# Kernel tuning notes

Hardware: AMD Instinct MI355X
Metric: run time of the kernel (lower is better)

Reference implementation:

```python
import jax, jax.numpy as jnp
import numpy as np

B, T = 2, 2048
D_MODEL, D_HIDDEN = 1024, 2048
N_EXPERTS, TOP_K = 8, 2
N_TOKENS = B * T
CAPACITY = 2 * N_TOKENS * TOP_K // N_EXPERTS  # 4096


def setup_inputs() -> dict:
    key = jax.random.key(0)
    k_x, k_rw, k_w, k_v, k_o = jax.random.split(key, 5)
    x = jax.random.normal(k_x, (B, T, D_MODEL), jnp.float32)
    # router: nn.Linear(d_model, n_experts) -> weight [E, D], bias [E]
    router_w = jax.random.normal(k_rw, (N_EXPERTS, D_MODEL), jnp.float32) * D_MODEL ** -0.5
    router_b = jnp.zeros((N_EXPERTS,), jnp.float32)
    # stacked expert params, matching SwiGLU init scales
    W = jax.random.normal(k_w, (N_EXPERTS, D_MODEL, D_HIDDEN), jnp.float32) * D_MODEL ** -0.5
    V = jax.random.normal(k_v, (N_EXPERTS, D_MODEL, D_HIDDEN), jnp.float32) * D_MODEL ** -0.5
    W_out = jax.random.normal(k_o, (N_EXPERTS, D_HIDDEN, D_MODEL), jnp.float32) * D_HIDDEN ** -0.5
    return {"x": x, "router_w": router_w, "router_b": router_b, "W": W, "V": V, "W_out": W_out}


def reference(x, router_w, router_b, W, V, W_out):
    Bq, Tq, D = x.shape
    N = Bq * Tq
    x_flat = x.reshape(N, D)

    # token-level top-k routing
    router_logits = x_flat @ router_w.T + router_b            # [N, E]
    top_vals, top_ids = jax.lax.top_k(router_logits, TOP_K)   # [N, K]
    top_probs = jax.nn.softmax(top_vals, axis=-1)             # [N, K]

    # pad row N: gathers with fill index N read zeros / contribute zero weight
    x_pad = jnp.concatenate([x_flat, jnp.zeros((1, D), x_flat.dtype)], axis=0)
    probs_pad = jnp.concatenate([top_probs, jnp.zeros((1, TOP_K), top_probs.dtype)], axis=0)

    out = jnp.zeros((N + 1, D), x_flat.dtype)
    for e in range(N_EXPERTS):  # static small loop over experts
        tok, slot = jnp.nonzero(top_ids == e, size=CAPACITY, fill_value=(N, 0))
        w = probs_pad[tok, slot][:, None]     # [C, 1], zero for padding slots
        xin = x_pad[tok]                      # [C, D] gather
        a = xin @ W[e]                        # [C, H]
        b = xin @ V[e]                        # [C, H]
        y = (a * (b * jax.nn.sigmoid(b))) @ W_out[e]  # SwiGLU: a * swish(b) -> [C, D]
        out = out.at[tok].add(y * w)          # weighted scatter-add
    return out[:N].reshape(Bq, Tq, D)
```

## Files before the change

kernel.cpp:

```cpp
#include <hip/hip_runtime.h>
#include <cstdint>
#include <cstddef>

#define N_TOK 4096
#define DM    1024
#define DH    2048
#define NE    8
#define NSLOT 8192

typedef short bf16x8_t __attribute__((ext_vector_type(8)));
typedef float f32x4    __attribute__((ext_vector_type(4)));
typedef unsigned short u16x8 __attribute__((ext_vector_type(8)));

__device__ __forceinline__ unsigned short f2bf(float f) {
  union { float f; unsigned int u; } v; v.f = f;
  unsigned int u = v.u;
  u += 0x7fffu + ((u >> 16) & 1u);
  return (unsigned short)(u >> 16);
}

__device__ __forceinline__ float bf2f(unsigned short h) {
  union { unsigned int u; float f; } v; v.u = ((unsigned int)h) << 16;
  return v.f;
}

#define GLD16(gp, lp)                                                          \
  __builtin_amdgcn_global_load_lds(                                            \
      (const __attribute__((address_space(1))) void*)(gp),                     \
      (__attribute__((address_space(3))) void*)(lp), 16, 0, 0)

__device__ __forceinline__ int expert_off(const int* __restrict__ counts, int e, int* cnt) {
  int off = 0, s = 0;
#pragma unroll
  for (int i = 0; i < NE; i++) { if (i == e) off = s; s += counts[i]; }
  *cnt = counts[e];
  return off;
}

__global__ __launch_bounds__(256) void k_transpose(
    const float* __restrict__ W, const float* __restrict__ V,
    const float* __restrict__ Wout, unsigned short* __restrict__ B1t,
    unsigned short* __restrict__ B2t, int* __restrict__ counts) {
  if (blockIdx.z == 0 && blockIdx.x == 0 && blockIdx.y == 0 && threadIdx.x < NE)
    counts[threadIdx.x] = 0;

  const int z = blockIdx.z;
  const float* s;
  unsigned short* d;
  int R, C, xt, yt;
  if (z < 16) {
    const int e = z & 7;
    s = ((z < 8) ? W : V) + (size_t)e * DM * DH;
    d = B1t + (size_t)e * 4096 * DM + (size_t)((z < 8) ? 0 : DH) * DM;
    R = DM; C = DH; xt = blockIdx.x; yt = blockIdx.y;
  } else {
    const int e = z - 16;
    s = Wout + (size_t)e * DH * DM;
    d = B2t + (size_t)e * DM * DH;
    R = DH; C = DM;
    const int flat = blockIdx.x * 16 + blockIdx.y;
    xt = flat & 15; yt = flat >> 4;
  }
  const int c0 = xt * 64, r0 = yt * 64;
  __shared__ float tile[64][65];
  const int t = threadIdx.x;
  {
    const int cc = (t & 15) * 4;
#pragma unroll
    for (int j = 0; j < 4; j++) {
      const int r = (t >> 4) + j * 16;
      const float4 v = *(const float4*)(s + (size_t)(r0 + r) * C + c0 + cc);
      tile[r][cc + 0] = v.x; tile[r][cc + 1] = v.y;
      tile[r][cc + 2] = v.z; tile[r][cc + 3] = v.w;
    }
  }
  __syncthreads();
  {
    const int r8 = (t & 7) * 8;
#pragma unroll
    for (int j = 0; j < 2; j++) {
      const int c = (t >> 3) + j * 32;
      u16x8 o;
#pragma unroll
      for (int i = 0; i < 8; i++) o[i] = f2bf(tile[r8 + i][c]);
      *(u16x8*)(d + (size_t)(c0 + c) * R + r0 + r8) = o;
    }
  }
}

__global__ __launch_bounds__(256) void k_router(
    const float* __restrict__ x, const float* __restrict__ rw,
    const float* __restrict__ rb, int* __restrict__ counts,
    int* __restrict__ meta_e, int* __restrict__ meta_idx,
    float* __restrict__ meta_p) {
  const int wv = threadIdx.x >> 6;
  const int l  = threadIdx.x & 63;
  const int tk = blockIdx.x * 4 + wv;
  const float* xr = x + (size_t)tk * DM;

  float acc[NE];
#pragma unroll
  for (int e = 0; e < NE; e++) acc[e] = 0.f;
#pragma unroll 4
  for (int i = 0; i < DM / 64; i++) {
    const float xv = xr[i * 64 + l];
#pragma unroll
    for (int e = 0; e < NE; e++) acc[e] += xv * rw[e * DM + i * 64 + l];
  }
#pragma unroll
  for (int off = 32; off > 0; off >>= 1) {
#pragma unroll
    for (int e = 0; e < NE; e++) acc[e] += __shfl_xor(acc[e], off);
  }
#pragma unroll
  for (int e = 0; e < NE; e++) acc[e] += rb[e];

  float v0 = -1e30f; int e0 = 0;
#pragma unroll
  for (int e = 0; e < NE; e++) { if (acc[e] > v0) { v0 = acc[e]; e0 = e; } }
  float v1 = -1e30f; int e1 = 0;
#pragma unroll
  for (int e = 0; e < NE; e++) { if (e != e0 && acc[e] > v1) { v1 = acc[e]; e1 = e; } }
  const float p0 = 1.0f / (1.0f + __expf(v1 - v0));
  const float p1 = 1.0f - p0;

  if (l == 0) {
    const int i0 = atomicAdd(&counts[e0], 1);
    const int i1 = atomicAdd(&counts[e1], 1);
    meta_e[tk * 2 + 0] = e0;  meta_e[tk * 2 + 1] = e1;
    meta_idx[tk * 2 + 0] = i0; meta_idx[tk * 2 + 1] = i1;
    meta_p[tk * 2 + 0] = p0;  meta_p[tk * 2 + 1] = p1;
  }
}

__global__ __launch_bounds__(256) void k_gather(
    const float* __restrict__ x, const int* __restrict__ meta_e,
    const int* __restrict__ meta_idx, const int* __restrict__ counts,
    unsigned short* __restrict__ Xg) {
  const int tk = blockIdx.x;
  int offs[NE];
  { int s = 0;
#pragma unroll
    for (int e = 0; e < NE; e++) { offs[e] = s; s += counts[e]; } }
  const int s0 = tk * 2, s1 = s0 + 1;
  const int g0 = offs[meta_e[s0]] + meta_idx[s0];
  const int g1 = offs[meta_e[s1]] + meta_idx[s1];
  const float4 v = ((const float4*)(x + (size_t)tk * DM))[threadIdx.x];
  ushort4 o;
  o.x = f2bf(v.x); o.y = f2bf(v.y); o.z = f2bf(v.z); o.w = f2bf(v.w);
  *(ushort4*)(Xg + (size_t)g0 * DM + threadIdx.x * 4) = o;
  *(ushort4*)(Xg + (size_t)g1 * DM + threadIdx.x * 4) = o;
}

__global__ __launch_bounds__(256, 2) void k_gemm1(
    const unsigned short* __restrict__ Xg, const unsigned short* __restrict__ B1t,
    unsigned short* __restrict__ G, const int* __restrict__ counts) {
  const int e = blockIdx.z;
  int cnt;
  const int off = expert_off(counts, e, &cnt);
  const int mt = blockIdx.y;
  if (mt * 128 >= cnt) return;
  const int h0 = blockIdx.x * 128;
  const int row_base = off + mt * 128;

  __shared__ unsigned short As[2][128 * 32];
  __shared__ unsigned short Ws[2][128 * 32];
  __shared__ unsigned short Vs[2][128 * 32];

  const int t = threadIdx.x;
  const int l = t & 63;
  const int w = t >> 6;
  const int wm = (w >> 1) * 64;
  const int wn = (w & 1) * 64;
  const int lr = l & 15;
  const int kq = (l >> 4) * 8;

  const unsigned short* Bw = B1t + ((size_t)e * 4096 + h0) * DM;
  const unsigned short* Bv = Bw + (size_t)DH * DM;

  const int c0 = t, c1 = t + 256;
  const int r0 = c0 >> 2, r1 = c1 >> 2;
  const int k0s = ((c0 & 3) ^ ((r0 >> 1) & 3)) << 3;
  const int k1s = ((c1 & 3) ^ ((r1 >> 1) & 3)) << 3;
  const size_t aoff0 = (size_t)min(row_base + r0, NSLOT - 1) * DM + k0s;
  const size_t aoff1 = (size_t)min(row_base + r1, NSLOT - 1) * DM + k1s;
  const size_t boff0 = (size_t)r0 * DM + k0s;
  const size_t boff1 = (size_t)r1 * DM + k1s;

#define STG1(buf, kk)                                                          \
  do {                                                                         \
    GLD16(Xg + aoff0 + (kk), &As[buf][c0 * 8]);                                \
    GLD16(Xg + aoff1 + (kk), &As[buf][c1 * 8]);                                \
    GLD16(Bw + boff0 + (kk), &Ws[buf][c0 * 8]);                                \
    GLD16(Bw + boff1 + (kk), &Ws[buf][c1 * 8]);                                \
    GLD16(Bv + boff0 + (kk), &Vs[buf][c0 * 8]);                                \
    GLD16(Bv + boff1 + (kk), &Vs[buf][c1 * 8]);                                \
  } while (0)

  f32x4 acc_a[4][4], acc_b[4][4];
  const f32x4 z4 = {0.f, 0.f, 0.f, 0.f};
#pragma unroll
  for (int i = 0; i < 4; i++)
#pragma unroll
    for (int j = 0; j < 4; j++) { acc_a[i][j] = z4; acc_b[i][j] = z4; }

  STG1(0, 0);
  __syncthreads();

  const int NS = DM / 32;
  for (int s = 0; s < NS; s++) {
    const int cur = s & 1;
    bf16x8_t af[4], wf[4], vf[4];
#pragma unroll
    for (int mi = 0; mi < 4; mi++) {
      const int row = wm + mi * 16 + lr;
      af[mi] = *(const bf16x8_t*)&As[cur][(row * 32 + kq) ^ (((row >> 1) & 3) << 3)];
    }
#pragma unroll
    for (int ni = 0; ni < 4; ni++) {
      const int row = wn + ni * 16 + lr;
      const int idx = (row * 32 + kq) ^ (((row >> 1) & 3) << 3);
      wf[ni] = *(const bf16x8_t*)&Ws[cur][idx];
      vf[ni] = *(const bf16x8_t*)&Vs[cur][idx];
    }
    if (s + 1 < NS) STG1(cur ^ 1, (s + 1) * 32);
#pragma unroll
    for (int mi = 0; mi < 4; mi++)
#pragma unroll
      for (int ni = 0; ni < 4; ni++) {
        acc_a[mi][ni] = __builtin_amdgcn_mfma_f32_16x16x32_bf16(af[mi], wf[ni], acc_a[mi][ni], 0, 0, 0);
        acc_b[mi][ni] = __builtin_amdgcn_mfma_f32_16x16x32_bf16(af[mi], vf[ni], acc_b[mi][ni], 0, 0, 0);
      }
    __syncthreads();
  }
#undef STG1

  const int q4 = (l >> 4) * 4;
#pragma unroll
  for (int mi = 0; mi < 4; mi++) {
#pragma unroll
    for (int r = 0; r < 4; r++) {
      const int mloc = mt * 128 + wm + mi * 16 + q4 + r;
      if (mloc >= cnt) continue;
      unsigned short* grow = G + (size_t)(off + mloc) * DH;
#pragma unroll
      for (int ni = 0; ni < 4; ni++) {
        const int h = h0 + wn + ni * 16 + lr;
        const float a = acc_a[mi][ni][r];
        const float b = acc_b[mi][ni][r];
        const float sgl = b / (1.0f + __expf(-b));
        grow[h] = f2bf(a * sgl);
      }
    }
  }
}

__global__ __launch_bounds__(256, 2) void k_gemm2(
    const unsigned short* __restrict__ G, const unsigned short* __restrict__ B2t,
    unsigned short* __restrict__ Y, const int* __restrict__ counts) {
  const int z = blockIdx.z;
  const int e = z & 7;
  const int half = z >> 3;
  int cnt;
  const int off = expert_off(counts, e, &cnt);
  const int mt = blockIdx.y;
  if (mt * 128 >= cnt) return;
  const int n0 = blockIdx.x * 128;
  const int row_base = off + mt * 128;
  const int kbase = half * 1024;

  __shared__ unsigned short As[2][128 * 32];
  __shared__ unsigned short Bs[2][128 * 32];

  const int t = threadIdx.x;
  const int l = t & 63;
  const int w = t >> 6;
  const int wm = (w >> 1) * 64;
  const int wn = (w & 1) * 64;
  const int lr = l & 15;
  const int kq = (l >> 4) * 8;

  const unsigned short* Bp = B2t + ((size_t)e * DM + n0) * DH;

  const int c0 = t, c1 = t + 256;
  const int r0 = c0 >> 2, r1 = c1 >> 2;
  const int k0s = ((c0 & 3) ^ ((r0 >> 1) & 3)) << 3;
  const int k1s = ((c1 & 3) ^ ((r1 >> 1) & 3)) << 3;
  const size_t aoff0 = (size_t)min(row_base + r0, NSLOT - 1) * DH + k0s;
  const size_t aoff1 = (size_t)min(row_base + r1, NSLOT - 1) * DH + k1s;
  const size_t boff0 = (size_t)r0 * DH + k0s;
  const size_t boff1 = (size_t)r1 * DH + k1s;

#define STG2(buf, kk)                                                          \
  do {                                                                         \
    GLD16(G + aoff0 + (kk), &As[buf][c0 * 8]);                                 \
    GLD16(G + aoff1 + (kk), &As[buf][c1 * 8]);                                 \
    GLD16(Bp + boff0 + (kk), &Bs[buf][c0 * 8]);                                \
    GLD16(Bp + boff1 + (kk), &Bs[buf][c1 * 8]);                                \
  } while (0)

  f32x4 acc[4][4];
  const f32x4 z4 = {0.f, 0.f, 0.f, 0.f};
#pragma unroll
  for (int i = 0; i < 4; i++)
#pragma unroll
    for (int j = 0; j < 4; j++) acc[i][j] = z4;

  STG2(0, kbase);
  __syncthreads();

  const int NS = 1024 / 32;
  for (int s = 0; s < NS; s++) {
    const int cur = s & 1;
    bf16x8_t af[4], bf[4];
#pragma unroll
    for (int mi = 0; mi < 4; mi++) {
      const int row = wm + mi * 16 + lr;
      af[mi] = *(const bf16x8_t*)&As[cur][(row * 32 + kq) ^ (((row >> 1) & 3) << 3)];
    }
#pragma unroll
    for (int ni = 0; ni < 4; ni++) {
      const int row = wn + ni * 16 + lr;
      bf[ni] = *(const bf16x8_t*)&Bs[cur][(row * 32 + kq) ^ (((row >> 1) & 3) << 3)];
    }
    if (s + 1 < NS) STG2(cur ^ 1, kbase + (s + 1) * 32);
#pragma unroll
    for (int mi = 0; mi < 4; mi++)
#pragma unroll
      for (int ni = 0; ni < 4; ni++)
        acc[mi][ni] = __builtin_amdgcn_mfma_f32_16x16x32_bf16(af[mi], bf[ni], acc[mi][ni], 0, 0, 0);
    __syncthreads();
  }
#undef STG2

  unsigned short* Yh = Y + (size_t)half * NSLOT * DM;
  const int q4 = (l >> 4) * 4;
#pragma unroll
  for (int mi = 0; mi < 4; mi++) {
#pragma unroll
    for (int r = 0; r < 4; r++) {
      const int mloc = mt * 128 + wm + mi * 16 + q4 + r;
      if (mloc >= cnt) continue;
      unsigned short* yrow = Yh + (size_t)(off + mloc) * DM;
#pragma unroll
      for (int ni = 0; ni < 4; ni++)
        yrow[n0 + wn + ni * 16 + lr] = f2bf(acc[mi][ni][r]);
    }
  }
}

__global__ __launch_bounds__(256) void k_combine(
    const unsigned short* __restrict__ Y, const int* __restrict__ meta_e,
    const int* __restrict__ meta_idx, const float* __restrict__ meta_p,
    const int* __restrict__ counts, float* __restrict__ out) {
  const int tk = blockIdx.x;
  int offs[NE];
  { int s = 0;
#pragma unroll
    for (int e = 0; e < NE; e++) { offs[e] = s; s += counts[e]; } }
  const int s0 = tk * 2, s1 = s0 + 1;
  const int g0 = offs[meta_e[s0]] + meta_idx[s0];
  const int g1 = offs[meta_e[s1]] + meta_idx[s1];
  const float w0 = meta_p[s0], w1 = meta_p[s1];
  const unsigned short* Y1 = Y + (size_t)NSLOT * DM;
  const ushort4 a0 = ((const ushort4*)(Y  + (size_t)g0 * DM))[threadIdx.x];
  const ushort4 a1 = ((const ushort4*)(Y1 + (size_t)g0 * DM))[threadIdx.x];
  const ushort4 b0 = ((const ushort4*)(Y  + (size_t)g1 * DM))[threadIdx.x];
  const ushort4 b1 = ((const ushort4*)(Y1 + (size_t)g1 * DM))[threadIdx.x];
  float4 o;
  o.x = w0 * (bf2f(a0.x) + bf2f(a1.x)) + w1 * (bf2f(b0.x) + bf2f(b1.x));
  o.y = w0 * (bf2f(a0.y) + bf2f(a1.y)) + w1 * (bf2f(b0.y) + bf2f(b1.y));
  o.z = w0 * (bf2f(a0.z) + bf2f(a1.z)) + w1 * (bf2f(b0.z) + bf2f(b1.z));
  o.w = w0 * (bf2f(a0.w) + bf2f(a1.w)) + w1 * (bf2f(b0.w) + bf2f(b1.w));
  ((float4*)(out + (size_t)tk * DM))[threadIdx.x] = o;
}

extern "C" void kernel_launch(void* const* d_in, const int* in_sizes, int n_in,
                              void* d_out, int out_size, void* d_ws, size_t ws_size,
                              hipStream_t stream) {
  const float* x    = (const float*)d_in[0];
  const float* rw   = (const float*)d_in[1];
  const float* rb   = (const float*)d_in[2];
  const float* W    = (const float*)d_in[3];
  const float* V    = (const float*)d_in[4];
  const float* Wout = (const float*)d_in[5];
  float* out = (float*)d_out;

  char* p = (char*)d_ws;
  unsigned short* B1t = (unsigned short*)p; p += (size_t)NE * 4096 * DM * 2;
  unsigned short* Y   = (unsigned short*)B1t;
  unsigned short* B2t = (unsigned short*)p; p += (size_t)NE * DM * DH * 2;
  unsigned short* Xg  = (unsigned short*)p; p += (size_t)NSLOT * DM * 2;
  unsigned short* G   = (unsigned short*)p; p += (size_t)NSLOT * DH * 2;
  int*   counts      = (int*)p;   p += 256;
  int*   meta_e      = (int*)p;   p += (size_t)N_TOK * 2 * 4;
  int*   meta_idx    = (int*)p;   p += (size_t)N_TOK * 2 * 4;
  float* meta_p      = (float*)p; p += (size_t)N_TOK * 2 * 4;

  k_transpose<<<dim3(32, 16, 24), 256, 0, stream>>>(W, V, Wout, B1t, B2t, counts);
  k_router<<<N_TOK / 4, 256, 0, stream>>>(x, rw, rb, counts, meta_e, meta_idx, meta_p);
  k_gather<<<N_TOK, 256, 0, stream>>>(x, meta_e, meta_idx, counts, Xg);
  k_gemm1<<<dim3(DH / 128, NSLOT / 128, NE), 256, 0, stream>>>(Xg, B1t, G, counts);
  k_gemm2<<<dim3(DM / 128, NSLOT / 128, 2 * NE), 256, 0, stream>>>(G, B2t, Y, counts);
  k_combine<<<N_TOK, 256, 0, stream>>>(Y, meta_e, meta_idx, meta_p, counts, out);
}
```

Measured before the change: 501.6 us.

## Use larger transpose tiles, block-local router atomics, and drop split-K in gemm2

The weight transpose kernel now handles 128x64 tiles per block, halving its grid. The router processes 32 tokens per block and aggregates per-expert counts in shared memory before one global atomic per expert, cutting global atomic contention. The second GEMM no longer splits K into two halves, so combine reads one partial output instead of two. This removes the extra Y traffic and the reduction, but halves gemm2's block count, which risks lower occupancy.

```diff
diff --git a/kernel.cpp b/kernel.cpp
--- a/kernel.cpp
+++ b/kernel.cpp
@@ -58,16 +58,16 @@
     s = Wout + (size_t)e * DH * DM;
     d = B2t + (size_t)e * DM * DH;
     R = DH; C = DM;
-    const int flat = blockIdx.x * 16 + blockIdx.y;
+    const int flat = blockIdx.x * 8 + blockIdx.y;
     xt = flat & 15; yt = flat >> 4;
   }
-  const int c0 = xt * 64, r0 = yt * 64;
-  __shared__ float tile[64][65];
+  const int c0 = xt * 64, r0 = yt * 128;
+  __shared__ float tile[128][65];
   const int t = threadIdx.x;
   {
     const int cc = (t & 15) * 4;
 #pragma unroll
-    for (int j = 0; j < 4; j++) {
+    for (int j = 0; j < 8; j++) {
       const int r = (t >> 4) + j * 16;
       const float4 v = *(const float4*)(s + (size_t)(r0 + r) * C + c0 + cc);
       tile[r][cc + 0] = v.x; tile[r][cc + 1] = v.y;
@@ -76,10 +76,11 @@
   }
   __syncthreads();
   {
-    const int r8 = (t & 7) * 8;
-#pragma unroll
-    for (int j = 0; j < 2; j++) {
-      const int c = (t >> 3) + j * 32;
+    const int r8 = (t & 15) * 8;
+    const int cb = t >> 4;
+#pragma unroll
+    for (int pass = 0; pass < 4; pass++) {
+      const int c = cb + pass * 16;
       u16x8 o;
 #pragma unroll
       for (int i = 0; i < 8; i++) o[i] = f2bf(tile[r8 + i][c]);
@@ -88,48 +89,73 @@
   }
 }
 
+#define RTR_TOK 32
 __global__ __launch_bounds__(256) void k_router(
     const float* __restrict__ x, const float* __restrict__ rw,
     const float* __restrict__ rb, int* __restrict__ counts,
     int* __restrict__ meta_e, int* __restrict__ meta_idx,
     float* __restrict__ meta_p) {
+  __shared__ int lcnt[NE];
+  __shared__ int lbase[NE];
+  __shared__ int   tokE[RTR_TOK][2];
+  __shared__ int   tokLi[RTR_TOK][2];
+  __shared__ float tokP[RTR_TOK][2];
+
   const int wv = threadIdx.x >> 6;
   const int l  = threadIdx.x & 63;
-  const int tk = blockIdx.x * 4 + wv;
-  const float* xr = x + (size_t)tk * DM;
-
-  float acc[NE];
-#pragma unroll
-  for (int e = 0; e < NE; e++) acc[e] = 0.f;
+  if (threadIdx.x < NE) lcnt[threadIdx.x] = 0;
+  __syncthreads();
+
+  for (int it = 0; it < RTR_TOK / 4; it++) {
+    const int lt = wv * (RTR_TOK / 4) + it;
+    const int tk = blockIdx.x * RTR_TOK + lt;
+    const float* xr = x + (size_t)tk * DM;
+
+    float acc[NE];
+#pragma unroll
+    for (int e = 0; e < NE; e++) acc[e] = 0.f;
 #pragma unroll 4
-  for (int i = 0; i < DM / 64; i++) {
-    const float xv = xr[i * 64 + l];
-#pragma unroll
-    for (int e = 0; e < NE; e++) acc[e] += xv * rw[e * DM + i * 64 + l];
-  }
-#pragma unroll
-  for (int off = 32; off > 0; off >>= 1) {
-#pragma unroll
-    for (int e = 0; e < NE; e++) acc[e] += __shfl_xor(acc[e], off);
-  }
-#pragma unroll
-  for (int e = 0; e < NE; e++) acc[e] += rb[e];
-
-  float v0 = -1e30f; int e0 = 0;
-#pragma unroll
-  for (int e = 0; e < NE; e++) { if (acc[e] > v0) { v0 = acc[e]; e0 = e; } }
-  float v1 = -1e30f; int e1 = 0;
-#pragma unroll
-  for (int e = 0; e < NE; e++) { if (e != e0 && acc[e] > v1) { v1 = acc[e]; e1 = e; } }
-  const float p0 = 1.0f / (1.0f + __expf(v1 - v0));
-  const float p1 = 1.0f - p0;
-
-  if (l == 0) {
-    const int i0 = atomicAdd(&counts[e0], 1);
-    const int i1 = atomicAdd(&counts[e1], 1);
-    meta_e[tk * 2 + 0] = e0;  meta_e[tk * 2 + 1] = e1;
-    meta_idx[tk * 2 + 0] = i0; meta_idx[tk * 2 + 1] = i1;
-    meta_p[tk * 2 + 0] = p0;  meta_p[tk * 2 + 1] = p1;
+    for (int i = 0; i < DM / 64; i++) {
+      const float xv = xr[i * 64 + l];
+#pragma unroll
+      for (int e = 0; e < NE; e++) acc[e] += xv * rw[e * DM + i * 64 + l];
+    }
+#pragma unroll
+    for (int off = 32; off > 0; off >>= 1) {
+#pragma unroll
+      for (int e = 0; e < NE; e++) acc[e] += __shfl_xor(acc[e], off);
+    }
+#pragma unroll
+    for (int e = 0; e < NE; e++) acc[e] += rb[e];
+
+    float v0 = -1e30f; int e0 = 0;
+#pragma unroll
+    for (int e = 0; e < NE; e++) { if (acc[e] > v0) { v0 = acc[e]; e0 = e; } }
+    float v1 = -1e30f; int e1 = 0;
+#pragma unroll
+    for (int e = 0; e < NE; e++) { if (e != e0 && acc[e] > v1) { v1 = acc[e]; e1 = e; } }
+    const float p0 = 1.0f / (1.0f + __expf(v1 - v0));
+    const float p1 = 1.0f - p0;
+
+    if (l == 0) {
+      const int li0 = atomicAdd(&lcnt[e0], 1);
+      const int li1 = atomicAdd(&lcnt[e1], 1);
+      tokE[lt][0] = e0;  tokE[lt][1] = e1;
+      tokLi[lt][0] = li0; tokLi[lt][1] = li1;
+      tokP[lt][0] = p0;  tokP[lt][1] = p1;
+    }
+  }
+  __syncthreads();
+  if (threadIdx.x < NE)
+    lbase[threadIdx.x] = atomicAdd(&counts[threadIdx.x], lcnt[threadIdx.x]);
+  __syncthreads();
+  if (threadIdx.x < RTR_TOK * 2) {
+    const int lt = threadIdx.x >> 1, k = threadIdx.x & 1;
+    const int tk = blockIdx.x * RTR_TOK + lt;
+    const int e = tokE[lt][k];
+    meta_e[tk * 2 + k] = e;
+    meta_idx[tk * 2 + k] = lbase[e] + tokLi[lt][k];
+    meta_p[tk * 2 + k] = tokP[lt][k];
   }
 }
 
@@ -258,16 +284,13 @@
 __global__ __launch_bounds__(256, 2) void k_gemm2(
     const unsigned short* __restrict__ G, const unsigned short* __restrict__ B2t,
     unsigned short* __restrict__ Y, const int* __restrict__ counts) {
-  const int z = blockIdx.z;
-  const int e = z & 7;
-  const int half = z >> 3;
+  const int e = blockIdx.z;
   int cnt;
   const int off = expert_off(counts, e, &cnt);
   const int mt = blockIdx.y;
   if (mt * 128 >= cnt) return;
   const int n0 = blockIdx.x * 128;
   const int row_base = off + mt * 128;
-  const int kbase = half * 1024;
 
   __shared__ unsigned short As[2][128 * 32];
   __shared__ unsigned short Bs[2][128 * 32];
@@ -306,10 +329,10 @@
 #pragma unroll
     for (int j = 0; j < 4; j++) acc[i][j] = z4;
 
-  STG2(0, kbase);
-  __syncthreads();
-
-  const int NS = 1024 / 32;
+  STG2(0, 0);
+  __syncthreads();
+
+  const int NS = DH / 32;
   for (int s = 0; s < NS; s++) {
     const int cur = s & 1;
     bf16x8_t af[4], bf[4];
@@ -323,7 +346,7 @@
       const int row = wn + ni * 16 + lr;
       bf[ni] = *(const bf16x8_t*)&Bs[cur][(row * 32 + kq) ^ (((row >> 1) & 3) << 3)];
     }
-    if (s + 1 < NS) STG2(cur ^ 1, kbase + (s + 1) * 32);
+    if (s + 1 < NS) STG2(cur ^ 1, (s + 1) * 32);
 #pragma unroll
     for (int mi = 0; mi < 4; mi++)
 #pragma unroll
@@ -333,7 +356,6 @@
   }
 #undef STG2
 
-  unsigned short* Yh = Y + (size_t)half * NSLOT * DM;
   const int q4 = (l >> 4) * 4;
 #pragma unroll
   for (int mi = 0; mi < 4; mi++) {
@@ -341,7 +363,7 @@
     for (int r = 0; r < 4; r++) {
       const int mloc = mt * 128 + wm + mi * 16 + q4 + r;
       if (mloc >= cnt) continue;
-      unsigned short* yrow = Yh + (size_t)(off + mloc) * DM;
+      unsigned short* yrow = Y + (size_t)(off + mloc) * DM;
 #pragma unroll
       for (int ni = 0; ni < 4; ni++)
         yrow[n0 + wn + ni * 16 + lr] = f2bf(acc[mi][ni][r]);
@@ -362,16 +384,13 @@
   const int g0 = offs[meta_e[s0]] + meta_idx[s0];
   const int g1 = offs[meta_e[s1]] + meta_idx[s1];
   const float w0 = meta_p[s0], w1 = meta_p[s1];
-  const unsigned short* Y1 = Y + (size_t)NSLOT * DM;
-  const ushort4 a0 = ((const ushort4*)(Y  + (size_t)g0 * DM))[threadIdx.x];
-  const ushort4 a1 = ((const ushort4*)(Y1 + (size_t)g0 * DM))[threadIdx.x];
-  const ushort4 b0 = ((const ushort4*)(Y  + (size_t)g1 * DM))[threadIdx.x];
-  const ushort4 b1 = ((const ushort4*)(Y1 + (size_t)g1 * DM))[threadIdx.x];
+  const ushort4 a0 = ((const ushort4*)(Y + (size_t)g0 * DM))[threadIdx.x];
+  const ushort4 b0 = ((const ushort4*)(Y + (size_t)g1 * DM))[threadIdx.x];
   float4 o;
-  o.x = w0 * (bf2f(a0.x) + bf2f(a1.x)) + w1 * (bf2f(b0.x) + bf2f(b1.x));
-  o.y = w0 * (bf2f(a0.y) + bf2f(a1.y)) + w1 * (bf2f(b0.y) + bf2f(b1.y));
-  o.z = w0 * (bf2f(a0.z) + bf2f(a1.z)) + w1 * (bf2f(b0.z) + bf2f(b1.z));
-  o.w = w0 * (bf2f(a0.w) + bf2f(a1.w)) + w1 * (bf2f(b0.w) + bf2f(b1.w));
+  o.x = w0 * bf2f(a0.x) + w1 * bf2f(b0.x);
+  o.y = w0 * bf2f(a0.y) + w1 * bf2f(b0.y);
+  o.z = w0 * bf2f(a0.z) + w1 * bf2f(b0.z);
+  o.w = w0 * bf2f(a0.w) + w1 * bf2f(b0.w);
   ((float4*)(out + (size_t)tk * DM))[threadIdx.x] = o;
 }
 
@@ -397,10 +416,10 @@
   int*   meta_idx    = (int*)p;   p += (size_t)N_TOK * 2 * 4;
   float* meta_p      = (float*)p; p += (size_t)N_TOK * 2 * 4;
 
-  k_transpose<<<dim3(32, 16, 24), 256, 0, stream>>>(W, V, Wout, B1t, B2t, counts);
-  k_router<<<N_TOK / 4, 256, 0, stream>>>(x, rw, rb, counts, meta_e, meta_idx, meta_p);
+  k_transpose<<<dim3(32, 8, 24), 256, 0, stream>>>(W, V, Wout, B1t, B2t, counts);
+  k_router<<<N_TOK / RTR_TOK, 256, 0, stream>>>(x, rw, rb, counts, meta_e, meta_idx, meta_p);
   k_gather<<<N_TOK, 256, 0, stream>>>(x, meta_e, meta_idx, counts, Xg);
   k_gemm1<<<dim3(DH / 128, NSLOT / 128, NE), 256, 0, stream>>>(Xg, B1t, G, counts);
-  k_gemm2<<<dim3(DM / 128, NSLOT / 128, 2 * NE), 256, 0, stream>>>(G, B2t, Y, counts);
+  k_gemm2<<<dim3(DM / 128, NSLOT / 128, NE), 256, 0, stream>>>(G, B2t, Y, counts);
   k_combine<<<N_TOK, 256, 0, stream>>>(Y, meta_e, meta_idx, meta_p, counts, out);
 }
```

Measured after the change: 442.5 us. 1.13x faster.
